# Optimization experiments

Hardware: AMD Instinct MI355X
Metric: run time of the kernel (lower is better)

The kernel has to match this reference:

```python
import jax, jax.numpy as jnp
import numpy as np

ALPHA = 0.2  # LeakyReLU negative slope
NEG_INF = -1e9


def setup_inputs() -> dict:
    key = jax.random.key(0)
    k1, k2, k3, k4 = jax.random.split(key, 4)
    B, N, Fin, Fout = 8, 2048, 128, 64
    h = jax.random.normal(k1, (B, N, Fin), dtype=jnp.float32)
    adj_mask = jax.random.randint(k2, (B, N, N), 0, 2).astype(jnp.int32)
    # xavier_uniform-style scales
    W = jax.random.uniform(k3, (Fout, Fin), dtype=jnp.float32,
                           minval=-1.0, maxval=1.0) * np.sqrt(6.0 / (Fin + Fout))
    a = jax.random.uniform(k4, (2 * Fout,), dtype=jnp.float32,
                           minval=-1.0, maxval=1.0) * np.sqrt(6.0 / (2 * Fout + 1))
    return {"h": h, "adj_mask": adj_mask, "W": W, "a": a}


def reference(h, adj_mask, W, a):
    # Wh: [B, N, Fout]
    Wh = jnp.einsum("bnf,of->bno", h, W)
    Fout = Wh.shape[-1]
    a1, a2 = a[:Fout], a[Fout:]
    # additive decomposition of a([Wh_i || Wh_j]): e_ij = leakyrelu(s1_i + s2_j)
    s1 = Wh @ a1  # [B, N]
    s2 = Wh @ a2  # [B, N]
    e = jax.nn.leaky_relu(s1[:, :, None] + s2[:, None, :], negative_slope=ALPHA)  # [B,N,N]
    e = jnp.where(adj_mask == 0, NEG_INF, e)
    attention = jax.nn.softmax(e, axis=-1)
    # dropout is identity in eval mode / p effectively 0 for the reference
    h_prime = jnp.einsum("bij,bjo->bio", attention, Wh)
    return h_prime
```

## Files before the change

kernel.cpp:

```cpp
#include <hip/hip_runtime.h>
#include <hip/hip_fp16.h>
#include <math.h>

#define LRELU_ALPHA 0.2f
#define NEG_INF -1000000000.0f
#define L2E 1.44269504088896340736f

constexpr int B_ = 8, N_ = 2048, FIN = 128, FOUT = 64;

typedef _Float16 __attribute__((ext_vector_type(8))) f16x8;
typedef float __attribute__((ext_vector_type(4))) f32x4;

__device__ __forceinline__ void gload16(const void* g, void* l) {
  __builtin_amdgcn_global_load_lds(
      (const __attribute__((address_space(1))) void*)g,
      (__attribute__((address_space(3))) void*)l, 16, 0, 0);
}

__global__ __launch_bounds__(256) void k_wh(
    const float* __restrict__ h, const float* __restrict__ W,
    const float* __restrict__ a, unsigned short* __restrict__ WhT,
    float* __restrict__ s1, float* __restrict__ s2) {
  __shared__ float Wt[128][65];
  __shared__ float hs[16][128];

  const int t = threadIdx.x;
  const int row0 = blockIdx.x * 16;

  for (int e = t; e < 64 * 128; e += 256) {
    int o = e >> 7, f = e & 127;
    Wt[f][o] = W[e];
  }
  {
    const float4* hg = (const float4*)(h + (size_t)row0 * FIN);
    for (int i4 = t; i4 < 16 * 32; i4 += 256) {
      int r = i4 >> 5, f4 = i4 & 31;
      *(float4*)&hs[r][f4 * 4] = hg[i4];
    }
  }
  __syncthreads();

  const int wave = t >> 6, lane = t & 63;
  float acc[4] = {0.f, 0.f, 0.f, 0.f};
#pragma unroll 4
  for (int f4 = 0; f4 < 32; ++f4) {
    float w0 = Wt[4 * f4 + 0][lane], w1 = Wt[4 * f4 + 1][lane];
    float w2 = Wt[4 * f4 + 2][lane], w3 = Wt[4 * f4 + 3][lane];
#pragma unroll
    for (int r = 0; r < 4; ++r) {
      float4 hv = *(const float4*)&hs[wave * 4 + r][f4 * 4];
      acc[r] += hv.x * w0 + hv.y * w1 + hv.z * w2 + hv.w * w3;
    }
  }

  const float a1v = a[lane], a2v = a[64 + lane];
  const int b = row0 / N_;
#pragma unroll
  for (int r = 0; r < 4; ++r) {
    const int row = row0 + wave * 4 + r;
    const int n = row - b * N_;
    const float v = acc[r];
    WhT[((size_t)b * 64 + lane) * N_ + n] = __half_as_ushort(__float2half(v));
    float p1 = v * a1v, p2 = v * a2v;
#pragma unroll
    for (int d = 32; d; d >>= 1) {
      p1 += __shfl_xor(p1, d, 64);
      p2 += __shfl_xor(p2, d, 64);
    }
    if (lane == 0) { s1[row] = p1; s2[row] = p2; }
  }
}

__global__ __launch_bounds__(256, 2) void k_attn(
    const unsigned short* __restrict__ WhT,
    const float* __restrict__ s1g, const float* __restrict__ s2g,
    const int* __restrict__ adj, float* __restrict__ out) {
  __shared__ __align__(16) unsigned char sbuf[4][16 * 1024];
  __shared__ float s2s[N_];

  const int t = threadIdx.x;
  const int wave = t >> 6, lane = t & 63;
  const int m = lane & 15, q = lane >> 4;
  const int b = blockIdx.y;
  const int i0 = blockIdx.x * 32;
  const int rg = wave & 1;
  const int p0 = (wave >> 1) * 2;

  const int* adjB = adj + (size_t)b * N_ * N_;
  const unsigned short* whB = WhT + (size_t)b * 64 * N_;

  {
    const float4* s2R = (const float4*)(s2g + (size_t)b * N_);
    for (int i = t; i < N_ / 4; i += 256) {
      float4 v = s2R[i];
      v.x *= L2E; v.y *= L2E; v.z *= L2E; v.w *= L2E;
      ((float4*)s2s)[i] = v;
    }
  }

  const float s1r = s1g[b * N_ + i0 + rg * 16 + m];
  const float c1 = (s1r - 2.0f) * L2E;
  const float c2 = (LRELU_ALPHA * s1r - 2.0f) * L2E;

  f16x8 ones;
#pragma unroll
  for (int j = 0; j < 8; ++j) ones[j] = (_Float16)1.0f;

  const unsigned char* gp[4];
  int gstr;
  if (wave < 2) {
    const size_t r = (size_t)(i0 + wave * 16 + m);
#pragma unroll
    for (int ii = 0; ii < 4; ++ii) {
      int ks = ii >> 1, hh = ii & 1;
      gp[ii] = (const unsigned char*)(adjB + r * N_ + ks * 32 + q * 8 + hh * 4);
    }
    gstr = 64 * 4;
  } else {
#pragma unroll
    for (int ii = 0; ii < 4; ++ii) {
      int g = (wave - 2) * 2 + (ii >> 1), ks = ii & 1;
      gp[ii] = (const unsigned char*)(whB + (size_t)(g * 16 + m) * N_ +
                                      ks * 32 + q * 8);
    }
    gstr = 64 * 2;
  }

#define STAGE(S, c)                                                       \
  {                                                                       \
    _Pragma("unroll") for (int ii = 0; ii < 4; ++ii)                      \
        gload16(gp[ii] + (size_t)(c) * gstr, (S) + (wave * 4 + ii) * 1024); \
  }

  f32x4 acc0 = {0.f, 0.f, 0.f, 0.f}, acc1 = acc0, accS = acc0;

  auto consume = [&](const unsigned char* base, int c) {
#pragma unroll
    for (int ks = 0; ks < 2; ++ks) {
      int4 A0 = *(const int4*)(base + (rg * 4 + ks * 2 + 0) * 1024 + lane * 16);
      int4 A1 = *(const int4*)(base + (rg * 4 + ks * 2 + 1) * 1024 + lane * 16);
      const float* sp = &s2s[c * 64 + ks * 32 + q * 8];
      float4 sv0 = *(const float4*)sp;
      float4 sv1 = *(const float4*)(sp + 4);
      float xs[8] = {sv0.x, sv0.y, sv0.z, sv0.w, sv1.x, sv1.y, sv1.z, sv1.w};
      int avs[8] = {A0.x, A0.y, A0.z, A0.w, A1.x, A1.y, A1.z, A1.w};
      f16x8 af;
#pragma unroll
      for (int j = 0; j < 8; ++j) {
        float x = xs[j];
        float e = fmaxf(c1 + x, fmaf(LRELU_ALPHA, x, c2));
        e = avs[j] ? e : NEG_INF;
        af[j] = (_Float16)__builtin_amdgcn_exp2f(e);
      }
      f16x8 b0 = *(const f16x8*)(base + (8 + (p0 + 0) * 2 + ks) * 1024 + lane * 16);
      f16x8 b1 = *(const f16x8*)(base + (8 + (p0 + 1) * 2 + ks) * 1024 + lane * 16);
      acc0 = __builtin_amdgcn_mfma_f32_16x16x32_f16(af, b0, acc0, 0, 0, 0);
      acc1 = __builtin_amdgcn_mfma_f32_16x16x32_f16(af, b1, acc1, 0, 0, 0);
      accS = __builtin_amdgcn_mfma_f32_16x16x32_f16(af, ones, accS, 0, 0, 0);
    }
  };

  STAGE(sbuf[0], 0)
  STAGE(sbuf[1], 1)
  STAGE(sbuf[2], 2)
  __syncthreads();

  consume(sbuf[0], 0);
  STAGE(sbuf[3], 3)

  for (int c = 1; c <= 28; ++c) {
    asm volatile("s_waitcnt vmcnt(8)" ::: "memory");
    __builtin_amdgcn_s_barrier();
    consume(sbuf[c & 3], c);
    STAGE(sbuf[(c + 3) & 3], c + 3)
  }
  asm volatile("s_waitcnt vmcnt(8)" ::: "memory");
  __builtin_amdgcn_s_barrier();
  consume(sbuf[1], 29);
  asm volatile("s_waitcnt vmcnt(4)" ::: "memory");
  __builtin_amdgcn_s_barrier();
  consume(sbuf[2], 30);
  asm volatile("s_waitcnt vmcnt(0)" ::: "memory");
  __builtin_amdgcn_s_barrier();
  consume(sbuf[3], 31);

#pragma unroll
  for (int r = 0; r < 4; ++r) {
    const int ri = q * 4 + r;
    const float l = accS[r];
    const float inv = (l == 0.f) ? 1.f : 1.f / l;
    const size_t row = (size_t)b * N_ + i0 + rg * 16 + ri;
    out[row * FOUT + (p0 + 0) * 16 + m] = acc0[r] * inv;
    out[row * FOUT + (p0 + 1) * 16 + m] = acc1[r] * inv;
  }
#undef STAGE
}

extern "C" void kernel_launch(void* const* d_in, const int* in_sizes, int n_in,
                              void* d_out, int out_size, void* d_ws, size_t ws_size,
                              hipStream_t stream) {
  const float* h   = (const float*)d_in[0];
  const int*   adj = (const int*)d_in[1];
  const float* W   = (const float*)d_in[2];
  const float* a   = (const float*)d_in[3];
  float* out = (float*)d_out;

  unsigned short* WhT = (unsigned short*)d_ws;
  float* s1 = (float*)(WhT + (size_t)B_ * 64 * N_);
  float* s2 = s1 + (size_t)B_ * N_;

  k_wh<<<dim3(B_ * N_ / 16), 256, 0, stream>>>(h, W, a, WhT, s1, s2);
  k_attn<<<dim3(N_ / 32, B_), 256, 0, stream>>>(WhT, s1, s2, adj, out);
}
```

Baseline: 222.5 us.

## Load adjacency directly into registers, stage only Wh through LDS

Adjacency mask tiles are now loaded by each wave straight from global memory into registers, using a three-deep register ring. They no longer go through LDS via global_load_lds, so only the WhT tiles are staged in LDS and the shared buffer is halved. This removes the LDS write and read round trip for the adjacency data, which is the dominant traffic. The cost is higher register pressure (12 int4 values) and redundant adjacency loads, since two waves share each row group. The vmcnt accounting also has to stay correct with the mixed load types.

```diff
diff --git a/kernel.cpp b/kernel.cpp
--- a/kernel.cpp
+++ b/kernel.cpp
@@ -75,7 +75,7 @@
     const unsigned short* __restrict__ WhT,
     const float* __restrict__ s1g, const float* __restrict__ s2g,
     const int* __restrict__ adj, float* __restrict__ out) {
-  __shared__ __align__(16) unsigned char sbuf[4][16 * 1024];
+  __shared__ __align__(16) unsigned char sbuf[4][8 * 1024];
   __shared__ float s2s[N_];
 
   const int t = threadIdx.x;
@@ -86,8 +86,8 @@
   const int rg = wave & 1;
   const int p0 = (wave >> 1) * 2;
 
-  const int* adjB = adj + (size_t)b * N_ * N_;
   const unsigned short* whB = WhT + (size_t)b * 64 * N_;
+  const int* adjR = adj + (size_t)b * N_ * N_ + (size_t)(i0 + rg * 16 + m) * N_;
 
   {
     const float4* s2R = (const float4*)(s2g + (size_t)b * N_);
@@ -106,83 +106,73 @@
 #pragma unroll
   for (int j = 0; j < 8; ++j) ones[j] = (_Float16)1.0f;
 
-  const unsigned char* gp[4];
-  int gstr;
-  if (wave < 2) {
-    const size_t r = (size_t)(i0 + wave * 16 + m);
-#pragma unroll
-    for (int ii = 0; ii < 4; ++ii) {
-      int ks = ii >> 1, hh = ii & 1;
-      gp[ii] = (const unsigned char*)(adjB + r * N_ + ks * 32 + q * 8 + hh * 4);
-    }
-    gstr = 64 * 4;
-  } else {
-#pragma unroll
-    for (int ii = 0; ii < 4; ++ii) {
-      int g = (wave - 2) * 2 + (ii >> 1), ks = ii & 1;
-      gp[ii] = (const unsigned char*)(whB + (size_t)(g * 16 + m) * N_ +
-                                      ks * 32 + q * 8);
-    }
-    gstr = 64 * 2;
-  }
-
-#define STAGE(S, c)                                                       \
-  {                                                                       \
-    _Pragma("unroll") for (int ii = 0; ii < 4; ++ii)                      \
-        gload16(gp[ii] + (size_t)(c) * gstr, (S) + (wave * 4 + ii) * 1024); \
-  }
-
+  const unsigned char* whP0 =
+      (const unsigned char*)(whB + (size_t)(wave * 16 + m) * N_ + q * 8);
+  const unsigned char* whP1 = whP0 + 64;
+
+#define STAGE(c)                                                            \
+  {                                                                         \
+    gload16(whP0 + (size_t)(c) * 128, &sbuf[(c) & 3][(wave * 2 + 0) * 1024]); \
+    gload16(whP1 + (size_t)(c) * 128, &sbuf[(c) & 3][(wave * 2 + 1) * 1024]); \
+  }
+#define ISSUE_ADJ(S, c)                 \
+  {                                     \
+    const int* ap = adjR + (c) * 64 + q * 8; \
+    S##0 = *(const int4*)(ap);          \
+    S##1 = *(const int4*)(ap + 4);      \
+    S##2 = *(const int4*)(ap + 32);     \
+    S##3 = *(const int4*)(ap + 36);     \
+  }
+#define CONSUME(S, c)                                                        \
+  {                                                                          \
+    const unsigned char* Bb = &sbuf[(c) & 3][0];                             \
+    _Pragma("unroll") for (int ks = 0; ks < 2; ++ks) {                       \
+      int4 A0 = ks ? S##2 : S##0;                                            \
+      int4 A1 = ks ? S##3 : S##1;                                            \
+      const float* sp = &s2s[(c) * 64 + ks * 32 + q * 8];                    \
+      float4 sv0 = *(const float4*)sp;                                       \
+      float4 sv1 = *(const float4*)(sp + 4);                                 \
+      float xs[8] = {sv0.x, sv0.y, sv0.z, sv0.w, sv1.x, sv1.y, sv1.z, sv1.w};\
+      int avs[8] = {A0.x, A0.y, A0.z, A0.w, A1.x, A1.y, A1.z, A1.w};         \
+      f16x8 af;                                                              \
+      _Pragma("unroll") for (int j = 0; j < 8; ++j) {                        \
+        float x = xs[j];                                                     \
+        float e = fmaxf(c1 + x, fmaf(LRELU_ALPHA, x, c2));                   \
+        e = avs[j] ? e : NEG_INF;                                            \
+        af[j] = (_Float16)__builtin_amdgcn_exp2f(e);        \
+      }                                                                      \
+      f16x8 b0 = *(const f16x8*)(Bb + ((p0 + 0) * 2 + ks) * 1024 + lane * 16);\
+      f16x8 b1 = *(const f16x8*)(Bb + ((p0 + 1) * 2 + ks) * 1024 + lane * 16);\
+      acc0 = __builtin_amdgcn_mfma_f32_16x16x32_f16(af, b0, acc0, 0, 0, 0);  \
+      acc1 = __builtin_amdgcn_mfma_f32_16x16x32_f16(af, b1, acc1, 0, 0, 0);  \
+      accS = __builtin_amdgcn_mfma_f32_16x16x32_f16(af, ones, accS, 0, 0, 0);\
+    }                                                                        \
+  }
+#define ITERX(c, S, VMS)                        \
+  {                                             \
+    asm volatile("s_waitcnt " VMS ::: "memory");\
+    __builtin_amdgcn_s_barrier();               \
+    CONSUME(S, c)                               \
+  }
+
+  int4 rA0, rA1, rA2, rA3, rB0, rB1, rB2, rB3, rC0, rC1, rC2, rC3;
   f32x4 acc0 = {0.f, 0.f, 0.f, 0.f}, acc1 = acc0, accS = acc0;
 
-  auto consume = [&](const unsigned char* base, int c) {
-#pragma unroll
-    for (int ks = 0; ks < 2; ++ks) {
-      int4 A0 = *(const int4*)(base + (rg * 4 + ks * 2 + 0) * 1024 + lane * 16);
-      int4 A1 = *(const int4*)(base + (rg * 4 + ks * 2 + 1) * 1024 + lane * 16);
-      const float* sp = &s2s[c * 64 + ks * 32 + q * 8];
-      float4 sv0 = *(const float4*)sp;
-      float4 sv1 = *(const float4*)(sp + 4);
-      float xs[8] = {sv0.x, sv0.y, sv0.z, sv0.w, sv1.x, sv1.y, sv1.z, sv1.w};
-      int avs[8] = {A0.x, A0.y, A0.z, A0.w, A1.x, A1.y, A1.z, A1.w};
-      f16x8 af;
-#pragma unroll
-      for (int j = 0; j < 8; ++j) {
-        float x = xs[j];
-        float e = fmaxf(c1 + x, fmaf(LRELU_ALPHA, x, c2));
-        e = avs[j] ? e : NEG_INF;
-        af[j] = (_Float16)__builtin_amdgcn_exp2f(e);
-      }
-      f16x8 b0 = *(const f16x8*)(base + (8 + (p0 + 0) * 2 + ks) * 1024 + lane * 16);
-      f16x8 b1 = *(const f16x8*)(base + (8 + (p0 + 1) * 2 + ks) * 1024 + lane * 16);
-      acc0 = __builtin_amdgcn_mfma_f32_16x16x32_f16(af, b0, acc0, 0, 0, 0);
-      acc1 = __builtin_amdgcn_mfma_f32_16x16x32_f16(af, b1, acc1, 0, 0, 0);
-      accS = __builtin_amdgcn_mfma_f32_16x16x32_f16(af, ones, accS, 0, 0, 0);
-    }
-  };
-
-  STAGE(sbuf[0], 0)
-  STAGE(sbuf[1], 1)
-  STAGE(sbuf[2], 2)
+  ISSUE_ADJ(rA, 0) STAGE(0)
+  ISSUE_ADJ(rB, 1) STAGE(1)
+  ISSUE_ADJ(rC, 2) STAGE(2)
   __syncthreads();
 
-  consume(sbuf[0], 0);
-  STAGE(sbuf[3], 3)
-
-  for (int c = 1; c <= 28; ++c) {
-    asm volatile("s_waitcnt vmcnt(8)" ::: "memory");
-    __builtin_amdgcn_s_barrier();
-    consume(sbuf[c & 3], c);
-    STAGE(sbuf[(c + 3) & 3], c + 3)
-  }
-  asm volatile("s_waitcnt vmcnt(8)" ::: "memory");
-  __builtin_amdgcn_s_barrier();
-  consume(sbuf[1], 29);
-  asm volatile("s_waitcnt vmcnt(4)" ::: "memory");
-  __builtin_amdgcn_s_barrier();
-  consume(sbuf[2], 30);
-  asm volatile("s_waitcnt vmcnt(0)" ::: "memory");
-  __builtin_amdgcn_s_barrier();
-  consume(sbuf[3], 31);
+  for (int cb = 0; cb < 27; cb += 3) {
+    ITERX(cb + 0, rA, "vmcnt(12)") ISSUE_ADJ(rA, cb + 3) STAGE(cb + 3)
+    ITERX(cb + 1, rB, "vmcnt(12)") ISSUE_ADJ(rB, cb + 4) STAGE(cb + 4)
+    ITERX(cb + 2, rC, "vmcnt(12)") ISSUE_ADJ(rC, cb + 5) STAGE(cb + 5)
+  }
+  ITERX(27, rA, "vmcnt(12)") ISSUE_ADJ(rA, 30) STAGE(30)
+  ITERX(28, rB, "vmcnt(12)") ISSUE_ADJ(rB, 31) STAGE(31)
+  ITERX(29, rC, "vmcnt(12)")
+  ITERX(30, rA, "vmcnt(6)")
+  ITERX(31, rB, "vmcnt(0)")
 
 #pragma unroll
   for (int r = 0; r < 4; ++r) {
@@ -194,6 +184,9 @@
     out[row * FOUT + (p0 + 1) * 16 + m] = acc1[r] * inv;
   }
 #undef STAGE
+#undef ISSUE_ADJ
+#undef CONSUME
+#undef ITERX
 }
 
 extern "C" void kernel_launch(void* const* d_in, const int* in_sizes, int n_in,
```

New measurement: 226.6 us. Within noise of the previous version (+1.8%).

## Shrink attention tile to 16 rows with double buffering for higher occupancy

Applied to the files above, without the earlier changes.

Each attention block now covers 16 query rows instead of 32, and each wave owns one 16-column output slice. The LDS ring drops from four 16KB stages to two 12KB stages, so the launch bound allows four blocks per CU instead of two. The grid is reordered with batch as the fastest-varying dimension. The trade-off is that every wave recomputes the exp/mask tile for the same 16 rows, which doubles the redundant exp work, and each WhT chunk is loaded twice as often. The shallower double-buffered pipeline also keeps less memory latency in flight per block.

```diff
diff --git a/kernel.cpp b/kernel.cpp
--- a/kernel.cpp
+++ b/kernel.cpp
@@ -71,20 +71,18 @@
   }
 }
 
-__global__ __launch_bounds__(256, 2) void k_attn(
+__global__ __launch_bounds__(256, 4) void k_attn(
     const unsigned short* __restrict__ WhT,
     const float* __restrict__ s1g, const float* __restrict__ s2g,
     const int* __restrict__ adj, float* __restrict__ out) {
-  __shared__ __align__(16) unsigned char sbuf[4][16 * 1024];
+  __shared__ __align__(16) unsigned char sbuf[2][12 * 1024];
   __shared__ float s2s[N_];
 
   const int t = threadIdx.x;
   const int wave = t >> 6, lane = t & 63;
   const int m = lane & 15, q = lane >> 4;
-  const int b = blockIdx.y;
-  const int i0 = blockIdx.x * 32;
-  const int rg = wave & 1;
-  const int p0 = (wave >> 1) * 2;
+  const int b = blockIdx.x;
+  const int i0 = blockIdx.y * 16;
 
   const int* adjB = adj + (size_t)b * N_ * N_;
   const unsigned short* whB = WhT + (size_t)b * 64 * N_;
@@ -98,7 +96,7 @@
     }
   }
 
-  const float s1r = s1g[b * N_ + i0 + rg * 16 + m];
+  const float s1r = s1g[b * N_ + i0 + m];
   const float c1 = (s1r - 2.0f) * L2E;
   const float c2 = (LRELU_ALPHA * s1r - 2.0f) * L2E;
 
@@ -106,39 +104,38 @@
 #pragma unroll
   for (int j = 0; j < 8; ++j) ones[j] = (_Float16)1.0f;
 
-  const unsigned char* gp[4];
-  int gstr;
-  if (wave < 2) {
-    const size_t r = (size_t)(i0 + wave * 16 + m);
-#pragma unroll
-    for (int ii = 0; ii < 4; ++ii) {
-      int ks = ii >> 1, hh = ii & 1;
-      gp[ii] = (const unsigned char*)(adjB + r * N_ + ks * 32 + q * 8 + hh * 4);
-    }
-    gstr = 64 * 4;
-  } else {
-#pragma unroll
-    for (int ii = 0; ii < 4; ++ii) {
-      int g = (wave - 2) * 2 + (ii >> 1), ks = ii & 1;
-      gp[ii] = (const unsigned char*)(whB + (size_t)(g * 16 + m) * N_ +
-                                      ks * 32 + q * 8);
-    }
-    gstr = 64 * 2;
-  }
-
-#define STAGE(S, c)                                                       \
-  {                                                                       \
-    _Pragma("unroll") for (int ii = 0; ii < 4; ++ii)                      \
-        gload16(gp[ii] + (size_t)(c) * gstr, (S) + (wave * 4 + ii) * 1024); \
-  }
-
-  f32x4 acc0 = {0.f, 0.f, 0.f, 0.f}, acc1 = acc0, accS = acc0;
+  const unsigned char* gp[3];
+  int gs[3];
+#pragma unroll
+  for (int s = 0; s < 3; ++s) {
+    const int j = wave * 3 + s;
+    if (j < 4) {
+      const int ks = j >> 1, hh = j & 1;
+      gp[s] = (const unsigned char*)(adjB + (size_t)(i0 + m) * N_ +
+                                     ks * 32 + q * 8 + hh * 4);
+      gs[s] = 64 * 4;
+    } else {
+      const int g = (j - 4) >> 1, ks = (j - 4) & 1;
+      gp[s] = (const unsigned char*)(whB + (size_t)(g * 16 + m) * N_ +
+                                     ks * 32 + q * 8);
+      gs[s] = 64 * 2;
+    }
+  }
+
+#define STAGE(S, c)                                                         \
+  {                                                                         \
+    _Pragma("unroll") for (int s = 0; s < 3; ++s)                           \
+        gload16(gp[s] + (size_t)(c) * gs[s],                                \
+                (S) + (wave * 3 + s) * 1024 + lane * 16);                   \
+  }
+
+  f32x4 acc = {0.f, 0.f, 0.f, 0.f}, accS = acc;
 
   auto consume = [&](const unsigned char* base, int c) {
 #pragma unroll
     for (int ks = 0; ks < 2; ++ks) {
-      int4 A0 = *(const int4*)(base + (rg * 4 + ks * 2 + 0) * 1024 + lane * 16);
-      int4 A1 = *(const int4*)(base + (rg * 4 + ks * 2 + 1) * 1024 + lane * 16);
+      int4 A0 = *(const int4*)(base + (ks * 2 + 0) * 1024 + lane * 16);
+      int4 A1 = *(const int4*)(base + (ks * 2 + 1) * 1024 + lane * 16);
       const float* sp = &s2s[c * 64 + ks * 32 + q * 8];
       float4 sv0 = *(const float4*)sp;
       float4 sv1 = *(const float4*)(sp + 4);
@@ -152,46 +149,35 @@
         e = avs[j] ? e : NEG_INF;
         af[j] = (_Float16)__builtin_amdgcn_exp2f(e);
       }
-      f16x8 b0 = *(const f16x8*)(base + (8 + (p0 + 0) * 2 + ks) * 1024 + lane * 16);
-      f16x8 b1 = *(const f16x8*)(base + (8 + (p0 + 1) * 2 + ks) * 1024 + lane * 16);
-      acc0 = __builtin_amdgcn_mfma_f32_16x16x32_f16(af, b0, acc0, 0, 0, 0);
-      acc1 = __builtin_amdgcn_mfma_f32_16x16x32_f16(af, b1, acc1, 0, 0, 0);
+      f16x8 bf =
+          *(const f16x8*)(base + (4 + wave * 2 + ks) * 1024 + lane * 16);
+      acc = __builtin_amdgcn_mfma_f32_16x16x32_f16(af, bf, acc, 0, 0, 0);
       accS = __builtin_amdgcn_mfma_f32_16x16x32_f16(af, ones, accS, 0, 0, 0);
     }
   };
 
   STAGE(sbuf[0], 0)
   STAGE(sbuf[1], 1)
-  STAGE(sbuf[2], 2)
   __syncthreads();
 
-  consume(sbuf[0], 0);
-  STAGE(sbuf[3], 3)
-
-  for (int c = 1; c <= 28; ++c) {
-    asm volatile("s_waitcnt vmcnt(8)" ::: "memory");
+  for (int c = 0; c < 30; ++c) {
+    consume(sbuf[c & 1], c);
     __builtin_amdgcn_s_barrier();
-    consume(sbuf[c & 3], c);
-    STAGE(sbuf[(c + 3) & 3], c + 3)
-  }
-  asm volatile("s_waitcnt vmcnt(8)" ::: "memory");
-  __builtin_amdgcn_s_barrier();
-  consume(sbuf[1], 29);
-  asm volatile("s_waitcnt vmcnt(4)" ::: "memory");
-  __builtin_amdgcn_s_barrier();
-  consume(sbuf[2], 30);
+    STAGE(sbuf[c & 1], c + 2)
+    asm volatile("s_waitcnt vmcnt(3)" ::: "memory");
+    __builtin_amdgcn_s_barrier();
+  }
+  consume(sbuf[0], 30);
   asm volatile("s_waitcnt vmcnt(0)" ::: "memory");
   __builtin_amdgcn_s_barrier();
-  consume(sbuf[3], 31);
+  consume(sbuf[1], 31);
 
 #pragma unroll
   for (int r = 0; r < 4; ++r) {
-    const int ri = q * 4 + r;
     const float l = accS[r];
     const float inv = (l == 0.f) ? 1.f : 1.f / l;
-    const size_t row = (size_t)b * N_ + i0 + rg * 16 + ri;
-    out[row * FOUT + (p0 + 0) * 16 + m] = acc0[r] * inv;
-    out[row * FOUT + (p0 + 1) * 16 + m] = acc1[r] * inv;
+    const size_t row = (size_t)b * N_ + i0 + q * 4 + r;
+    out[row * FOUT + wave * 16 + m] = acc[r] * inv;
   }
 #undef STAGE
 }
@@ -210,5 +196,5 @@
   float* s2 = s1 + (size_t)B_ * N_;
 
   k_wh<<<dim3(B_ * N_ / 16), 256, 0, stream>>>(h, W, a, WhT, s1, s2);
-  k_attn<<<dim3(N_ / 32, B_), 256, 0, stream>>>(WhT, s1, s2, adj, out);
-}
+  k_attn<<<dim3(B_, N_ / 16), 256, 0, stream>>>(WhT, s1, s2, adj, out);
+}
```

Result: slower. 236.5 us (+6.3%).
